# Kernel tuning notes

Measured on AMD Instinct MI355X. Metric: run time of the kernel, lower is better.

Reference implementation:

```python
import jax, jax.numpy as jnp
import numpy as np

N, D = 8192, 1024

def setup_inputs() -> dict:
    key = jax.random.key(0)
    k1, k2 = jax.random.split(key)
    query = jax.random.normal(k1, (N, D), dtype=jnp.float32)
    keys = jax.random.normal(k2, (N, D), dtype=jnp.float32)
    return {"query": query, "keys": keys}

def reference(query, keys):
    # raw_attention[i] = <query[i], keys[i]>  -> shape [n]
    raw = jnp.sum(query * keys, axis=1)
    # original: materialize diag(raw) [n,n], softmax over the diagonal entries,
    # scatter back; off-diagonal entries are zeros. Equivalent to diag(softmax(raw)).
    sm = jax.nn.softmax(raw, axis=0)
    return jnp.diag(sm)  # [n, n]
```

## Files before the change

### kernel.cpp

```cpp
#include <hip/hip_runtime.h>
#include <math.h>

#define N 8192
#define D 1024

__global__ __launch_bounds__(256) void dot_rows(const float* __restrict__ q,
                                                const float* __restrict__ k,
                                                float* __restrict__ raw) {
    const int wave = threadIdx.x >> 6;
    const int lane = threadIdx.x & 63;
    const int row  = blockIdx.x * 4 + wave;
    const float4* q4 = (const float4*)(q + (size_t)row * D);
    const float4* k4 = (const float4*)(k + (size_t)row * D);
    float s = 0.f;
    #pragma unroll
    for (int i = 0; i < 4; ++i) {
        float4 a = q4[lane + 64 * i];
        float4 b = k4[lane + 64 * i];
        s += a.x * b.x + a.y * b.y + a.z * b.z + a.w * b.w;
    }
    #pragma unroll
    for (int off = 32; off; off >>= 1) s += __shfl_down(s, off, 64);
    if (lane == 0) raw[row] = s;
}

__global__ __launch_bounds__(1024) void softmax_scatter(const float* __restrict__ raw,
                                                        float* __restrict__ out) {
    const int t    = threadIdx.x;
    const int lane = t & 63;
    const int wid  = t >> 6;
    __shared__ float red[16];

    float v[8];
    float m = -INFINITY;
    #pragma unroll
    for (int i = 0; i < 8; ++i) {
        v[i] = raw[t + 1024 * i];
        m = fmaxf(m, v[i]);
    }
    #pragma unroll
    for (int off = 32; off; off >>= 1) m = fmaxf(m, __shfl_down(m, off, 64));
    if (lane == 0) red[wid] = m;
    __syncthreads();
    if (wid == 0) {
        float mm = (lane < 16) ? red[lane] : -INFINITY;
        #pragma unroll
        for (int off = 8; off; off >>= 1) mm = fmaxf(mm, __shfl_down(mm, off, 64));
        if (lane == 0) red[0] = mm;
    }
    __syncthreads();
    m = red[0];
    __syncthreads();

    float s = 0.f;
    #pragma unroll
    for (int i = 0; i < 8; ++i) {
        v[i] = __expf(v[i] - m);
        s += v[i];
    }
    #pragma unroll
    for (int off = 32; off; off >>= 1) s += __shfl_down(s, off, 64);
    if (lane == 0) red[wid] = s;
    __syncthreads();
    if (wid == 0) {
        float ss = (lane < 16) ? red[lane] : 0.f;
        #pragma unroll
        for (int off = 8; off; off >>= 1) ss += __shfl_down(ss, off, 64);
        if (lane == 0) red[0] = ss;
    }
    __syncthreads();
    const float inv = 1.0f / red[0];
    #pragma unroll
    for (int i = 0; i < 8; ++i) {
        const int row = t + 1024 * i;
        out[(size_t)row * (N + 1)] = v[i] * inv;
    }
}

extern "C" void kernel_launch(void* const* d_in, const int* in_sizes, int n_in,
                              void* d_out, int out_size, void* d_ws, size_t ws_size,
                              hipStream_t stream) {
    const float* q = (const float*)d_in[0];
    const float* k = (const float*)d_in[1];
    float* out = (float*)d_out;
    float* raw = (float*)d_ws;

    hipMemsetAsync(out, 0, (size_t)N * N * sizeof(float), stream);
    dot_rows<<<N / 4, 256, 0, stream>>>(q, k, raw);
    softmax_scatter<<<1, 1024, 0, stream>>>(raw, out);
}
```

Measured before the change: 72.22 us.

## Fuse zero-fill with softmax scatter and skip diagonal in fill

Drops the separate full-matrix memset. The second kernel now does two jobs: block 0 computes the softmax and writes the diagonal, and 2048 other blocks zero-fill four rows each with nontemporal vector stores. The fill blocks skip the diagonal slots, so the two writers never race and the single-block softmax runs alongside the fill instead of after it. In exchange, the softmax block now uses 256 threads and computes exp twice per element, and the fill relies on a hand-written store loop rather than the driver memset.

```diff
diff --git a/kernel.cpp b/kernel.cpp
--- a/kernel.cpp
+++ b/kernel.cpp
@@ -3,6 +3,8 @@
 
 #define N 8192
 #define D 1024
+
+typedef float f32x4 __attribute__((ext_vector_type(4)));
 
 __global__ __launch_bounds__(256) void dot_rows(const float* __restrict__ q,
                                                 const float* __restrict__ k,
@@ -24,56 +26,57 @@
     if (lane == 0) raw[row] = s;
 }
 
-__global__ __launch_bounds__(1024) void softmax_scatter(const float* __restrict__ raw,
+__global__ __launch_bounds__(256) void fill_and_softmax(const float* __restrict__ raw,
                                                         float* __restrict__ out) {
-    const int t    = threadIdx.x;
-    const int lane = t & 63;
-    const int wid  = t >> 6;
-    __shared__ float red[16];
+    const int bid = blockIdx.x;
+    const int t   = threadIdx.x;
 
-    float v[8];
-    float m = -INFINITY;
-    #pragma unroll
-    for (int i = 0; i < 8; ++i) {
-        v[i] = raw[t + 1024 * i];
-        m = fmaxf(m, v[i]);
-    }
-    #pragma unroll
-    for (int off = 32; off; off >>= 1) m = fmaxf(m, __shfl_down(m, off, 64));
-    if (lane == 0) red[wid] = m;
-    __syncthreads();
-    if (wid == 0) {
-        float mm = (lane < 16) ? red[lane] : -INFINITY;
+    if (bid == 0) {
+        const int lane = t & 63;
+        const int wid  = t >> 6;
+        __shared__ float red[4];
+
+        float m = -INFINITY;
         #pragma unroll
-        for (int off = 8; off; off >>= 1) mm = fmaxf(mm, __shfl_down(mm, off, 64));
-        if (lane == 0) red[0] = mm;
-    }
-    __syncthreads();
-    m = red[0];
-    __syncthreads();
+        for (int i = 0; i < 32; ++i) m = fmaxf(m, raw[t + 256 * i]);
+        #pragma unroll
+        for (int off = 32; off; off >>= 1) m = fmaxf(m, __shfl_down(m, off, 64));
+        if (lane == 0) red[wid] = m;
+        __syncthreads();
+        m = fmaxf(fmaxf(red[0], red[1]), fmaxf(red[2], red[3]));
+        __syncthreads();
 
-    float s = 0.f;
-    #pragma unroll
-    for (int i = 0; i < 8; ++i) {
-        v[i] = __expf(v[i] - m);
-        s += v[i];
-    }
-    #pragma unroll
-    for (int off = 32; off; off >>= 1) s += __shfl_down(s, off, 64);
-    if (lane == 0) red[wid] = s;
-    __syncthreads();
-    if (wid == 0) {
-        float ss = (lane < 16) ? red[lane] : 0.f;
+        float s = 0.f;
         #pragma unroll
-        for (int off = 8; off; off >>= 1) ss += __shfl_down(ss, off, 64);
-        if (lane == 0) red[0] = ss;
-    }
-    __syncthreads();
-    const float inv = 1.0f / red[0];
-    #pragma unroll
-    for (int i = 0; i < 8; ++i) {
-        const int row = t + 1024 * i;
-        out[(size_t)row * (N + 1)] = v[i] * inv;
+        for (int i = 0; i < 32; ++i) s += __expf(raw[t + 256 * i] - m);
+        #pragma unroll
+        for (int off = 32; off; off >>= 1) s += __shfl_down(s, off, 64);
+        if (lane == 0) red[wid] = s;
+        __syncthreads();
+        const float inv = 1.0f / (red[0] + red[1] + red[2] + red[3]);
+
+        #pragma unroll
+        for (int i = 0; i < 32; ++i) {
+            const int r = t + 256 * i;
+            out[(size_t)r * (N + 1)] = __expf(raw[r] - m) * inv;
+        }
+    } else {
+        const int fb = bid - 1;
+        f32x4* o4 = (f32x4*)out + (size_t)fb * 8192;
+        const f32x4 z = {0.f, 0.f, 0.f, 0.f};
+        #pragma unroll
+        for (int i = 0; i < 32; ++i) {
+            const int g = t + 256 * i;
+            if ((g & 2047) == fb) {
+                const int j = g >> 11;
+                float* w = (float*)(o4 + g);
+                #pragma unroll
+                for (int c = 0; c < 4; ++c)
+                    if (c != j) __builtin_nontemporal_store(0.f, w + c);
+            } else {
+                __builtin_nontemporal_store(z, o4 + g);
+            }
+        }
     }
 }
 
@@ -85,7 +88,6 @@
     float* out = (float*)d_out;
     float* raw = (float*)d_ws;
 
-    hipMemsetAsync(out, 0, (size_t)N * N * sizeof(float), stream);
     dot_rows<<<N / 4, 256, 0, stream>>>(q, k, raw);
-    softmax_scatter<<<1, 1024, 0, stream>>>(raw, out);
+    fill_and_softmax<<<N / 4 + 1, 256, 0, stream>>>(raw, out);
 }
```

Measured after the change: 66.62 us. -7.8%, faster.
